# Performance work log

Measured on AMD Instinct MI355X. Metric: run time of the kernel, lower is better.

The kernel has to match this reference:

```python
import jax, jax.numpy as jnp
import numpy as np

NUM_HEADS = 8  # matches init_kwargs num_heads
LN_EPS = 1e-5  # torch.nn.LayerNorm default


def setup_inputs() -> dict:
    key = jax.random.key(0)
    ks = jax.random.split(key, 12)
    E, B, H, S = 16384, 16, 256, 32
    edge_features = jax.random.normal(ks[0], (E, H), jnp.float32)
    edge_coords = jax.random.normal(ks[1], (E, 3), jnp.float32)
    # sorted, equal-size segments (all graphs non-empty)
    batch = jnp.repeat(jnp.arange(B, dtype=jnp.int32), E // B)
    s_h = 1.0 / np.sqrt(H)
    s_sh = 1.0 / np.sqrt(S * H)
    seed_vectors = jax.random.normal(ks[2], (S, H), jnp.float32)
    # weights stored [in, out] (transposed vs torch nn.Linear)
    Wq = jax.random.normal(ks[3], (H, H), jnp.float32) * s_h
    Wk = jax.random.normal(ks[4], (H, H), jnp.float32) * s_h
    Wv = jax.random.normal(ks[5], (H, H), jnp.float32) * s_h
    Wo = jax.random.normal(ks[6], (H, H), jnp.float32) * s_h
    bo = jnp.zeros((H,), jnp.float32)
    ln_g = jnp.ones((H,), jnp.float32)
    ln_b = jnp.zeros((H,), jnp.float32)
    W1 = jax.random.normal(ks[7], (S * H, H), jnp.float32) * s_sh
    b1 = jnp.zeros((H,), jnp.float32)
    W2 = jax.random.normal(ks[8], (H, H), jnp.float32) * s_h
    b2 = jnp.zeros((H,), jnp.float32)
    return dict(edge_features=edge_features, edge_coords=edge_coords, batch=batch,
                seed_vectors=seed_vectors, Wq=Wq, Wk=Wk, Wv=Wv, Wo=Wo, bo=bo,
                ln_g=ln_g, ln_b=ln_b, W1=W1, b1=b1, W2=W2, b2=b2, num_graphs=B)


def reference(edge_features, edge_coords, batch, seed_vectors, Wq, Wk, Wv, Wo, bo,
              ln_g, ln_b, W1, b1, W2, b2, num_graphs):
    S, H = seed_vectors.shape
    nh = NUM_HEADS
    hd = H // nh
    q = (seed_vectors @ Wq).reshape(S, nh, hd)          # shared across graphs
    k = (edge_features @ Wk).reshape(-1, nh, hd)        # [E, nh, hd]
    v = (edge_features @ Wv).reshape(-1, nh, hd)
    scores = jnp.einsum('shd,ehd->esh', q, k) / np.sqrt(hd).astype(np.float32)
    # segment softmax over edges within each graph
    m = jax.lax.stop_gradient(jax.ops.segment_max(scores, batch, num_segments=num_graphs))
    num = jnp.exp(scores - m[batch])
    den = jax.ops.segment_sum(num, batch, num_segments=num_graphs)
    w = num / den[batch]                                # [E, S, nh]
    att = jax.ops.segment_sum(jnp.einsum('esh,ehd->eshd', w, v), batch,
                              num_segments=num_graphs)  # [B, S, nh, hd]
    att = att.reshape(num_graphs, S, H)                 # concat heads (head-major)
    y = seed_vectors[None, :, :] + att @ Wo + bo        # residual + out_proj
    mu = jnp.mean(y, axis=-1, keepdims=True)
    var = jnp.mean((y - mu) ** 2, axis=-1, keepdims=True)
    y = (y - mu) / jnp.sqrt(var + LN_EPS) * ln_g + ln_b
    flat = y.reshape(num_graphs, S * H)
    h1 = jax.nn.silu(flat @ W1 + b1)
    return h1 @ W2 + b2                                 # [B, H]
```

## Files before the change

### kernel.cpp

```cpp
#include <hip/hip_runtime.h>
#include <math.h>
#include <stdint.h>

#define E_EDGES 16384
#define H_DIM   256
#define S_SEEDS 32
#define NHEADS  8
#define HDIM    32
#define BGRAPHS 16
#define EPG     1024
#define N2      512
#define RSQRT_HD 0.17677669529663687f

typedef __attribute__((ext_vector_type(8))) short bf16x8;
typedef __attribute__((ext_vector_type(4))) float f32x4;

__device__ inline unsigned short f2bf(float x) {
    unsigned u = __float_as_uint(x);
    u += 0x7fff + ((u >> 16) & 1);
    return (unsigned short)(u >> 16);
}
__device__ inline float bf2f(unsigned int h) {
    return __uint_as_float((h & 0xffffu) << 16);
}

__global__ __launch_bounds__(256) void k_wc(const float* __restrict__ Wv,
                                            const float* __restrict__ Wk,
                                            const float* __restrict__ Wq,
                                            const float* __restrict__ seed,
                                            unsigned short* __restrict__ WcT) {
    int j = blockIdx.x;
    int i = threadIdx.x;
    float val;
    if (j < H_DIM) {
        val = Wv[i * H_DIM + j];
    } else {
        int c = j - H_DIM;
        int h = c >> 5, s = c & 31;
        __shared__ float qp[8][33];
        __shared__ float qrow[HDIM];
        int d = i & 31, g = i >> 5;
        const float* wq = &Wq[(g * 32) * H_DIM + h * HDIM + d];
        const float* sd = &seed[s * H_DIM + g * 32];
        float p = 0.f;
        #pragma unroll
        for (int ii = 0; ii < 32; ++ii)
            p = fmaf(sd[ii], wq[(size_t)ii * H_DIM], p);
        qp[g][d] = p;
        __syncthreads();
        if (i < HDIM) {
            float qv = 0.f;
            #pragma unroll
            for (int g2 = 0; g2 < 8; ++g2) qv += qp[g2][i];
            qrow[i] = qv;
        }
        __syncthreads();
        const float* wk = &Wk[i * H_DIM + h * HDIM];
        float acc = 0.f;
        #pragma unroll
        for (int dd = 0; dd < HDIM; dd += 4) {
            float4 w = *(const float4*)&wk[dd];
            float4 qq = *(const float4*)&qrow[dd];
            acc = fmaf(w.x, qq.x, acc); acc = fmaf(w.y, qq.y, acc);
            acc = fmaf(w.z, qq.z, acc); acc = fmaf(w.w, qq.w, acc);
        }
        val = acc * RSQRT_HD;
    }
    WcT[j * H_DIM + i] = f2bf(val);
}

__global__ __launch_bounds__(256) void k_convA(const float* __restrict__ A,
                                               unsigned short* __restrict__ Abf) {
    size_t idx = (size_t)blockIdx.x * 256 + threadIdx.x;
    const float4* src = (const float4*)A;
    float4 a = src[idx * 2], b = src[idx * 2 + 1];
    uint4 o;
    o.x = (unsigned)f2bf(a.x) | ((unsigned)f2bf(a.y) << 16);
    o.y = (unsigned)f2bf(a.z) | ((unsigned)f2bf(a.w) << 16);
    o.z = (unsigned)f2bf(b.x) | ((unsigned)f2bf(b.y) << 16);
    o.w = (unsigned)f2bf(b.z) | ((unsigned)f2bf(b.w) << 16);
    ((uint4*)Abf)[idx] = o;
}

#define BKP 40
__global__ __launch_bounds__(256) void k_gemm(const unsigned short* __restrict__ Abf,
                                              const unsigned short* __restrict__ WcT,
                                              unsigned short* __restrict__ C,
                                              float* __restrict__ pmax,
                                              float* __restrict__ psum) {
    __shared__ unsigned short As[128][BKP];
    __shared__ unsigned short Bs[128][BKP];
    __shared__ float smx[2][128];
    __shared__ float ssm[2][128];
    int tid = threadIdx.x;
    int e0 = blockIdx.x * 128, n0 = blockIdx.y * 128;
    int w = tid >> 6, lane = tid & 63;
    int wm = (w >> 1) * 64, wn = (w & 1) * 64;
    int lr = lane & 15, kg = lane >> 4;
    int srow = tid >> 1;
    int scol = (tid & 1) * 16;
    f32x4 acc[4][4] = {};
    for (int k0 = 0; k0 < H_DIM; k0 += 32) {
        const unsigned short* ap = &Abf[(size_t)(e0 + srow) * H_DIM + k0 + scol];
        const unsigned short* bp = &WcT[(size_t)(n0 + srow) * H_DIM + k0 + scol];
        uint4 av0 = *(const uint4*)(ap);
        uint4 av1 = *(const uint4*)(ap + 8);
        uint4 bv0 = *(const uint4*)(bp);
        uint4 bv1 = *(const uint4*)(bp + 8);
        __syncthreads();
        *(uint4*)&As[srow][scol]     = av0;
        *(uint4*)&As[srow][scol + 8] = av1;
        *(uint4*)&Bs[srow][scol]     = bv0;
        *(uint4*)&Bs[srow][scol + 8] = bv1;
        __syncthreads();
        bf16x8 af[4], bfv[4];
        #pragma unroll
        for (int mi = 0; mi < 4; ++mi)
            af[mi] = *(const bf16x8*)&As[wm + mi * 16 + lr][kg * 8];
        #pragma unroll
        for (int ni = 0; ni < 4; ++ni)
            bfv[ni] = *(const bf16x8*)&Bs[wn + ni * 16 + lr][kg * 8];
        #pragma unroll
        for (int mi = 0; mi < 4; ++mi)
            #pragma unroll
            for (int ni = 0; ni < 4; ++ni)
                acc[mi][ni] = __builtin_amdgcn_mfma_f32_16x16x32_bf16(af[mi], bfv[ni], acc[mi][ni], 0, 0, 0);
    }
    if (n0 >= H_DIM) {
        #pragma unroll
        for (int mi = 0; mi < 4; ++mi)
            #pragma unroll
            for (int ni = 0; ni < 4; ++ni)
                #pragma unroll
                for (int r = 0; r < 4; ++r)
                    acc[mi][ni][r] = bf2f(f2bf(acc[mi][ni][r]));
        float tmax[4];
        #pragma unroll
        for (int ni = 0; ni < 4; ++ni) {
            float m = -1e30f;
            #pragma unroll
            for (int mi = 0; mi < 4; ++mi)
                #pragma unroll
                for (int r = 0; r < 4; ++r) m = fmaxf(m, acc[mi][ni][r]);
            m = fmaxf(m, __shfl_xor(m, 16, 64));
            m = fmaxf(m, __shfl_xor(m, 32, 64));
            tmax[ni] = m;
        }
        if (kg == 0) {
            #pragma unroll
            for (int ni = 0; ni < 4; ++ni) smx[w >> 1][wn + ni * 16 + lr] = tmax[ni];
        }
        __syncthreads();
        float csum[4];
        #pragma unroll
        for (int ni = 0; ni < 4; ++ni) {
            int col = wn + ni * 16 + lr;
            float m = fmaxf(smx[0][col], smx[1][col]);
            float s = 0.f;
            #pragma unroll
            for (int mi = 0; mi < 4; ++mi)
                #pragma unroll
                for (int r = 0; r < 4; ++r) s += __expf(acc[mi][ni][r] - m);
            s += __shfl_xor(s, 16, 64);
            s += __shfl_xor(s, 32, 64);
            csum[ni] = s;
        }
        if (kg == 0) {
            #pragma unroll
            for (int ni = 0; ni < 4; ++ni) ssm[w >> 1][wn + ni * 16 + lr] = csum[ni];
        }
        __syncthreads();
        if (tid < 128) {
            float m = fmaxf(smx[0][tid], smx[1][tid]);
            float s = ssm[0][tid] + ssm[1][tid];
            int gcol = (n0 - H_DIM) + tid;
            pmax[(size_t)blockIdx.x * H_DIM + gcol] = m;
            psum[(size_t)blockIdx.x * H_DIM + gcol] = s;
        }
    }
    #pragma unroll
    for (int mi = 0; mi < 4; ++mi)
        #pragma unroll
        for (int ni = 0; ni < 4; ++ni)
            #pragma unroll
            for (int r = 0; r < 4; ++r) {
                int e = e0 + wm + mi * 16 + kg * 4 + r;
                int n = n0 + wn + ni * 16 + lr;
                C[(size_t)e * N2 + n] = f2bf(acc[mi][ni][r]);
            }
}

__global__ __launch_bounds__(256) void k_wsum(const unsigned short* __restrict__ C,
                                              const float* __restrict__ pmax,
                                              const float* __restrict__ psum,
                                              float* __restrict__ patt) {
    int b = blockIdx.x, h = blockIdx.y, eq = blockIdx.z;
    int t = threadIdx.x;
    int s = t & 31, dg = t >> 5;
    __shared__ float pbuf[128][33];
    __shared__ float ml[32], il[32];
    if (t < 32) {
        int col = h * 32 + t;
        float m = -1e30f;
        #pragma unroll
        for (int j = 0; j < 8; ++j)
            m = fmaxf(m, pmax[(size_t)(b * 8 + j) * H_DIM + col]);
        float sm = 0.f;
        #pragma unroll
        for (int j = 0; j < 8; ++j)
            sm += psum[(size_t)(b * 8 + j) * H_DIM + col] *
                  __expf(pmax[(size_t)(b * 8 + j) * H_DIM + col] - m);
        ml[t] = m; il[t] = 1.f / sm;
    }
    __syncthreads();
    int e0 = b * EPG + eq * 128;
    #pragma unroll
    for (int ii = 0; ii < 16; ++ii) {
        int el = dg + 8 * ii;
        float x = bf2f(C[(size_t)(e0 + el) * N2 + H_DIM + h * 32 + s]);
        pbuf[el][s] = __expf(x - ml[s]) * il[s];
    }
    __syncthreads();
    float a0 = 0.f, a1 = 0.f, a2 = 0.f, a3 = 0.f;
    for (int el = 0; el < 128; ++el) {
        uint2 vv = *(const uint2*)&C[(size_t)(e0 + el) * N2 + h * 32 + dg * 4];
        float p = pbuf[el][s];
        a0 = fmaf(p, bf2f(vv.x), a0);
        a1 = fmaf(p, bf2f(vv.x >> 16), a1);
        a2 = fmaf(p, bf2f(vv.y), a2);
        a3 = fmaf(p, bf2f(vv.y >> 16), a3);
    }
    float4 o = {a0, a1, a2, a3};
    *(float4*)&patt[(size_t)((eq * 16 + b) * 32 + s) * H_DIM + h * 32 + dg * 4] = o;
}

__device__ inline float block_sum256(float v, float* red4) {
    for (int o = 32; o > 0; o >>= 1) v += __shfl_xor(v, o, 64);
    int wid = threadIdx.x >> 6;
    if ((threadIdx.x & 63) == 0) red4[wid] = v;
    __syncthreads();
    float r = red4[0] + red4[1] + red4[2] + red4[3];
    __syncthreads();
    return r;
}

__global__ __launch_bounds__(256) void k_proj_ln(const float* __restrict__ patt,
                                                 const float* __restrict__ seed,
                                                 const float* __restrict__ Wo,
                                                 const float* __restrict__ bo,
                                                 const float* __restrict__ ln_g,
                                                 const float* __restrict__ ln_b,
                                                 float* __restrict__ Y) {
    int bs0 = blockIdx.x * 4;
    int c = threadIdx.x;
    __shared__ float arow[4][H_DIM];
    __shared__ float red4[4];
    #pragma unroll
    for (int r = 0; r < 4; ++r) {
        int bs = bs0 + r;
        int b = bs >> 5, s = bs & 31;
        float a = 0.f;
        #pragma unroll
        for (int eq = 0; eq < 8; ++eq)
            a += patt[(size_t)((eq * 16 + b) * 32 + s) * H_DIM + c];
        arow[r][c] = a;
    }
    __syncthreads();
    float acc[4];
    float b0 = bo[c];
    #pragma unroll
    for (int r = 0; r < 4; ++r) acc[r] = b0;
    for (int i = 0; i < H_DIM; i += 4) {
        float4 a0 = *(const float4*)&arow[0][i];
        float4 a1 = *(const float4*)&arow[1][i];
        float4 a2 = *(const float4*)&arow[2][i];
        float4 a3 = *(const float4*)&arow[3][i];
        float w0 = Wo[(i + 0) * H_DIM + c], w1 = Wo[(i + 1) * H_DIM + c];
        float w2 = Wo[(i + 2) * H_DIM + c], w3 = Wo[(i + 3) * H_DIM + c];
        acc[0] = fmaf(a0.x, w0, acc[0]); acc[0] = fmaf(a0.y, w1, acc[0]);
        acc[0] = fmaf(a0.z, w2, acc[0]); acc[0] = fmaf(a0.w, w3, acc[0]);
        acc[1] = fmaf(a1.x, w0, acc[1]); acc[1] = fmaf(a1.y, w1, acc[1]);
        acc[1] = fmaf(a1.z, w2, acc[1]); acc[1] = fmaf(a1.w, w3, acc[1]);
        acc[2] = fmaf(a2.x, w0, acc[2]); acc[2] = fmaf(a2.y, w1, acc[2]);
        acc[2] = fmaf(a2.z, w2, acc[2]); acc[2] = fmaf(a2.w, w3, acc[2]);
        acc[3] = fmaf(a3.x, w0, acc[3]); acc[3] = fmaf(a3.y, w1, acc[3]);
        acc[3] = fmaf(a3.z, w2, acc[3]); acc[3] = fmaf(a3.w, w3, acc[3]);
    }
    float g = ln_g[c], be = ln_b[c];
    #pragma unroll
    for (int r = 0; r < 4; ++r) {
        int bs = bs0 + r;
        float y = seed[(bs & 31) * H_DIM + c] + acc[r];
        float mu = block_sum256(y, red4) * (1.f / 256.f);
        float d = y - mu;
        float var = block_sum256(d * d, red4) * (1.f / 256.f);
        Y[(size_t)bs * H_DIM + c] = d * rsqrtf(var + 1e-5f) * g + be;
    }
}

__global__ __launch_bounds__(256) void k_mlp1(const float* __restrict__ Y,
                                              const float* __restrict__ W1,
                                              float* __restrict__ part) {
    int ch = blockIdx.x;
    int c = threadIdx.x;
    int i0 = ch * 64;
    __shared__ float fbuf[16][64];
    #pragma unroll
    for (int it = 0; it < 4; ++it) {
        int li = it * 256 + c;
        fbuf[li >> 6][li & 63] = Y[(size_t)(li >> 6) * 8192 + i0 + (li & 63)];
    }
    __syncthreads();
    float acc[16];
    #pragma unroll
    for (int b = 0; b < 16; ++b) acc[b] = 0.f;
    for (int ii = 0; ii < 64; ++ii) {
        float w = W1[(size_t)(i0 + ii) * H_DIM + c];
        #pragma unroll
        for (int b = 0; b < 16; ++b) acc[b] = fmaf(fbuf[b][ii], w, acc[b]);
    }
    #pragma unroll
    for (int b = 0; b < 16; ++b)
        part[((size_t)b * 128 + ch) * H_DIM + c] = acc[b];
}

__global__ __launch_bounds__(256) void k_mlp2(const float* __restrict__ part,
                                              const float* __restrict__ b1,
                                              const float* __restrict__ W2,
                                              const float* __restrict__ b2,
                                              float* __restrict__ out) {
    int b = blockIdx.x;
    int c = threadIdx.x;
    float s = b1[c];
    const float* pb = &part[(size_t)b * 128 * H_DIM + c];
    #pragma unroll 4
    for (int ch = 0; ch < 128; ++ch) s += pb[(size_t)ch * H_DIM];
    float h1 = s / (1.f + __expf(-s));
    __shared__ float hrow[H_DIM];
    hrow[c] = h1;
    __syncthreads();
    float acc = b2[c];
    for (int j = 0; j < H_DIM; j += 4) {
        float4 hq = *(const float4*)&hrow[j];
        acc = fmaf(hq.x, W2[(j + 0) * H_DIM + c], acc);
        acc = fmaf(hq.y, W2[(j + 1) * H_DIM + c], acc);
        acc = fmaf(hq.z, W2[(j + 2) * H_DIM + c], acc);
        acc = fmaf(hq.w, W2[(j + 3) * H_DIM + c], acc);
    }
    out[(size_t)b * H_DIM + c] = acc;
}

extern "C" void kernel_launch(void* const* d_in, const int* in_sizes, int n_in,
                              void* d_out, int out_size, void* d_ws, size_t ws_size,
                              hipStream_t stream) {
    const float* edge_features = (const float*)d_in[0];
    const float* seed = (const float*)d_in[3];
    const float* Wq   = (const float*)d_in[4];
    const float* Wk   = (const float*)d_in[5];
    const float* Wv   = (const float*)d_in[6];
    const float* Wo   = (const float*)d_in[7];
    const float* bo   = (const float*)d_in[8];
    const float* ln_g = (const float*)d_in[9];
    const float* ln_b = (const float*)d_in[10];
    const float* W1   = (const float*)d_in[11];
    const float* b1   = (const float*)d_in[12];
    const float* W2   = (const float*)d_in[13];
    const float* b2   = (const float*)d_in[14];
    float* out = (float*)d_out;

    float* ws = (float*)d_ws;
    unsigned short* WcT  = (unsigned short*)ws;
    unsigned short* C    = WcT + 512 * H_DIM;
    float*          post = (float*)(C + (size_t)E_EDGES * N2);
    unsigned short* Abf  = (unsigned short*)post;
    float* pmax = post;
    float* psum = pmax + 32768;
    float* patt = psum + 32768;
    float* Y    = patt + 1048576;
    float* part = Y + 131072;

    k_wc       <<<N2, 256, 0, stream>>>(Wv, Wk, Wq, seed, WcT);
    k_convA    <<<E_EDGES * H_DIM / (256 * 8), 256, 0, stream>>>(edge_features, Abf);
    k_gemm     <<<dim3(E_EDGES / 128, N2 / 128), 256, 0, stream>>>(Abf, WcT, C, pmax, psum);
    k_wsum     <<<dim3(BGRAPHS, NHEADS, 8), 256, 0, stream>>>(C, pmax, psum, patt);
    k_proj_ln  <<<BGRAPHS * S_SEEDS / 4, 256, 0, stream>>>(patt, seed, Wo, bo, ln_g, ln_b, Y);
    k_mlp1     <<<128, 256, 0, stream>>>(Y, W1, part);
    k_mlp2     <<<BGRAPHS, 256, 0, stream>>>(part, b1, W2, b2, out);
}
```

Before: 166.6 us.

## Fuse fp32-to-bf16 conversion into GEMM and stage wsum tiles through LDS

Removes the separate k_convA kernel: the GEMM now loads fp32 edge features directly and converts them to bf16 while staging into shared memory. This drops one launch and the write and re-read of the bf16 copy of A, at the cost of reading 4-byte elements four times over, since each A tile is loaded by each of the four column blocks. k_wsum now loads score and value tiles into LDS with coalesced 16-byte loads, where before it did strided global reads per edge. Each block covers two 128-edge chunks, so the partial count drops from 8 to 4 and k_proj_ln sums fewer partials.

```diff
diff --git a/kernel.cpp b/kernel.cpp
--- a/kernel.cpp
+++ b/kernel.cpp
@@ -22,6 +22,9 @@
 }
 __device__ inline float bf2f(unsigned int h) {
     return __uint_as_float((h & 0xffffu) << 16);
+}
+__device__ inline unsigned pack2(float a, float b) {
+    return (unsigned)f2bf(a) | ((unsigned)f2bf(b) << 16);
 }
 
 __global__ __launch_bounds__(256) void k_wc(const float* __restrict__ Wv,
@@ -69,21 +72,8 @@
     WcT[j * H_DIM + i] = f2bf(val);
 }
 
-__global__ __launch_bounds__(256) void k_convA(const float* __restrict__ A,
-                                               unsigned short* __restrict__ Abf) {
-    size_t idx = (size_t)blockIdx.x * 256 + threadIdx.x;
-    const float4* src = (const float4*)A;
-    float4 a = src[idx * 2], b = src[idx * 2 + 1];
-    uint4 o;
-    o.x = (unsigned)f2bf(a.x) | ((unsigned)f2bf(a.y) << 16);
-    o.y = (unsigned)f2bf(a.z) | ((unsigned)f2bf(a.w) << 16);
-    o.z = (unsigned)f2bf(b.x) | ((unsigned)f2bf(b.y) << 16);
-    o.w = (unsigned)f2bf(b.z) | ((unsigned)f2bf(b.w) << 16);
-    ((uint4*)Abf)[idx] = o;
-}
-
 #define BKP 40
-__global__ __launch_bounds__(256) void k_gemm(const unsigned short* __restrict__ Abf,
+__global__ __launch_bounds__(256) void k_gemm(const float* __restrict__ A,
                                               const unsigned short* __restrict__ WcT,
                                               unsigned short* __restrict__ C,
                                               float* __restrict__ pmax,
@@ -101,12 +91,19 @@
     int scol = (tid & 1) * 16;
     f32x4 acc[4][4] = {};
     for (int k0 = 0; k0 < H_DIM; k0 += 32) {
-        const unsigned short* ap = &Abf[(size_t)(e0 + srow) * H_DIM + k0 + scol];
+        const float* ap = &A[(size_t)(e0 + srow) * H_DIM + k0 + scol];
+        float4 a0 = *(const float4*)(ap);
+        float4 a1 = *(const float4*)(ap + 4);
+        float4 a2 = *(const float4*)(ap + 8);
+        float4 a3 = *(const float4*)(ap + 12);
         const unsigned short* bp = &WcT[(size_t)(n0 + srow) * H_DIM + k0 + scol];
-        uint4 av0 = *(const uint4*)(ap);
-        uint4 av1 = *(const uint4*)(ap + 8);
         uint4 bv0 = *(const uint4*)(bp);
         uint4 bv1 = *(const uint4*)(bp + 8);
+        uint4 av0, av1;
+        av0.x = pack2(a0.x, a0.y); av0.y = pack2(a0.z, a0.w);
+        av0.z = pack2(a1.x, a1.y); av0.w = pack2(a1.z, a1.w);
+        av1.x = pack2(a2.x, a2.y); av1.y = pack2(a2.z, a2.w);
+        av1.z = pack2(a3.x, a3.y); av1.w = pack2(a3.z, a3.w);
         __syncthreads();
         *(uint4*)&As[srow][scol]     = av0;
         *(uint4*)&As[srow][scol + 8] = av1;
@@ -156,14 +153,14 @@
         for (int ni = 0; ni < 4; ++ni) {
             int col = wn + ni * 16 + lr;
             float m = fmaxf(smx[0][col], smx[1][col]);
-            float s = 0.f;
+            float sv = 0.f;
             #pragma unroll
             for (int mi = 0; mi < 4; ++mi)
                 #pragma unroll
-                for (int r = 0; r < 4; ++r) s += __expf(acc[mi][ni][r] - m);
-            s += __shfl_xor(s, 16, 64);
-            s += __shfl_xor(s, 32, 64);
-            csum[ni] = s;
+                for (int r = 0; r < 4; ++r) sv += __expf(acc[mi][ni][r] - m);
+            sv += __shfl_xor(sv, 16, 64);
+            sv += __shfl_xor(sv, 32, 64);
+            csum[ni] = sv;
         }
         if (kg == 0) {
             #pragma unroll
@@ -172,10 +169,10 @@
         __syncthreads();
         if (tid < 128) {
             float m = fmaxf(smx[0][tid], smx[1][tid]);
-            float s = ssm[0][tid] + ssm[1][tid];
+            float sv = ssm[0][tid] + ssm[1][tid];
             int gcol = (n0 - H_DIM) + tid;
             pmax[(size_t)blockIdx.x * H_DIM + gcol] = m;
-            psum[(size_t)blockIdx.x * H_DIM + gcol] = s;
+            psum[(size_t)blockIdx.x * H_DIM + gcol] = sv;
         }
     }
     #pragma unroll
@@ -190,13 +187,16 @@
             }
 }
 
+#define VSP 40
 __global__ __launch_bounds__(256) void k_wsum(const unsigned short* __restrict__ C,
                                               const float* __restrict__ pmax,
                                               const float* __restrict__ psum,
                                               float* __restrict__ patt) {
-    int b = blockIdx.x, h = blockIdx.y, eq = blockIdx.z;
+    int b = blockIdx.x, h = blockIdx.y, pp = blockIdx.z;
     int t = threadIdx.x;
     int s = t & 31, dg = t >> 5;
+    __shared__ unsigned short sbuf[128][VSP];
+    __shared__ unsigned short vbuf[128][VSP];
     __shared__ float pbuf[128][33];
     __shared__ float ml[32], il[32];
     if (t < 32) {
@@ -212,26 +212,40 @@
                   __expf(pmax[(size_t)(b * 8 + j) * H_DIM + col] - m);
         ml[t] = m; il[t] = 1.f / sm;
     }
-    __syncthreads();
-    int e0 = b * EPG + eq * 128;
-    #pragma unroll
-    for (int ii = 0; ii < 16; ++ii) {
-        int el = dg + 8 * ii;
-        float x = bf2f(C[(size_t)(e0 + el) * N2 + H_DIM + h * 32 + s]);
-        pbuf[el][s] = __expf(x - ml[s]) * il[s];
-    }
-    __syncthreads();
+    int r = t >> 1, halfo = (t & 1) * 16;
     float a0 = 0.f, a1 = 0.f, a2 = 0.f, a3 = 0.f;
-    for (int el = 0; el < 128; ++el) {
-        uint2 vv = *(const uint2*)&C[(size_t)(e0 + el) * N2 + h * 32 + dg * 4];
-        float p = pbuf[el][s];
-        a0 = fmaf(p, bf2f(vv.x), a0);
-        a1 = fmaf(p, bf2f(vv.x >> 16), a1);
-        a2 = fmaf(p, bf2f(vv.y), a2);
-        a3 = fmaf(p, bf2f(vv.y >> 16), a3);
+    for (int ch = 0; ch < 2; ++ch) {
+        int e0 = b * EPG + (pp * 2 + ch) * 128;
+        const unsigned short* crow = &C[(size_t)(e0 + r) * N2 + h * 32 + halfo];
+        uint4 sv0 = *(const uint4*)(crow + H_DIM);
+        uint4 sv1 = *(const uint4*)(crow + H_DIM + 8);
+        uint4 vv0 = *(const uint4*)(crow);
+        uint4 vv1 = *(const uint4*)(crow + 8);
+        __syncthreads();
+        *(uint4*)&sbuf[r][halfo]     = sv0;
+        *(uint4*)&sbuf[r][halfo + 8] = sv1;
+        *(uint4*)&vbuf[r][halfo]     = vv0;
+        *(uint4*)&vbuf[r][halfo + 8] = vv1;
+        __syncthreads();
+        #pragma unroll
+        for (int ii = 0; ii < 16; ++ii) {
+            int el = dg + 8 * ii;
+            float x = bf2f(sbuf[el][s]);
+            pbuf[el][s] = __expf(x - ml[s]) * il[s];
+        }
+        __syncthreads();
+        #pragma unroll 16
+        for (int el = 0; el < 128; ++el) {
+            float p = pbuf[el][s];
+            uint2 vv = *(const uint2*)&vbuf[el][dg * 4];
+            a0 = fmaf(p, bf2f(vv.x), a0);
+            a1 = fmaf(p, bf2f(vv.x >> 16), a1);
+            a2 = fmaf(p, bf2f(vv.y), a2);
+            a3 = fmaf(p, bf2f(vv.y >> 16), a3);
+        }
     }
     float4 o = {a0, a1, a2, a3};
-    *(float4*)&patt[(size_t)((eq * 16 + b) * 32 + s) * H_DIM + h * 32 + dg * 4] = o;
+    *(float4*)&patt[(size_t)((pp * 16 + b) * 32 + s) * H_DIM + h * 32 + dg * 4] = o;
 }
 
 __device__ inline float block_sum256(float v, float* red4) {
@@ -261,7 +275,7 @@
         int b = bs >> 5, s = bs & 31;
         float a = 0.f;
         #pragma unroll
-        for (int eq = 0; eq < 8; ++eq)
+        for (int eq = 0; eq < 4; ++eq)
             a += patt[(size_t)((eq * 16 + b) * 32 + s) * H_DIM + c];
         arow[r][c] = a;
     }
@@ -371,18 +385,15 @@
     float* ws = (float*)d_ws;
     unsigned short* WcT  = (unsigned short*)ws;
     unsigned short* C    = WcT + 512 * H_DIM;
-    float*          post = (float*)(C + (size_t)E_EDGES * N2);
-    unsigned short* Abf  = (unsigned short*)post;
-    float* pmax = post;
+    float* pmax = (float*)(C + (size_t)E_EDGES * N2);
     float* psum = pmax + 32768;
     float* patt = psum + 32768;
-    float* Y    = patt + 1048576;
+    float* Y    = patt + 524288;
     float* part = Y + 131072;
 
     k_wc       <<<N2, 256, 0, stream>>>(Wv, Wk, Wq, seed, WcT);
-    k_convA    <<<E_EDGES * H_DIM / (256 * 8), 256, 0, stream>>>(edge_features, Abf);
-    k_gemm     <<<dim3(E_EDGES / 128, N2 / 128), 256, 0, stream>>>(Abf, WcT, C, pmax, psum);
-    k_wsum     <<<dim3(BGRAPHS, NHEADS, 8), 256, 0, stream>>>(C, pmax, psum, patt);
+    k_gemm     <<<dim3(E_EDGES / 128, N2 / 128), 256, 0, stream>>>(edge_features, WcT, C, pmax, psum);
+    k_wsum     <<<dim3(BGRAPHS, NHEADS, 4), 256, 0, stream>>>(C, pmax, psum, patt);
     k_proj_ln  <<<BGRAPHS * S_SEEDS / 4, 256, 0, stream>>>(patt, seed, Wo, bo, ln_g, ln_b, Y);
     k_mlp1     <<<128, 256, 0, stream>>>(Y, W1, part);
     k_mlp2     <<<BGRAPHS, 256, 0, stream>>>(part, b1, W2, b2, out);
```

Measured after the change: 158.8 us. -4.7%, faster.
